# Kernel tuning notes

Measured on AMD Instinct MI355X. Metric: run time of the kernel, lower is better.

Reference implementation:

```python
import jax, jax.numpy as jnp
import numpy as np

SEQ, BATCH, EMBED = 1024, 2, 768
E = 16            # num_experts = m * N = 2 * 8
FFN_H = 1536      # expert_dim = ceil(3072 / 2)
K_SHARED = 1
K_ROUTE = 3       # (m * top_k) - k_shared = 4 - 1
LN_EPS = 1e-5
NEG_INF = -1e9


def setup_inputs() -> dict:
    key = jax.random.key(0)
    ks = jax.random.split(key, 4)
    x = jax.random.normal(ks[0], (SEQ, BATCH, EMBED), dtype=jnp.float32)
    gate_w = jax.random.normal(ks[1], (EMBED, E), dtype=jnp.float32) * 0.02
    gate_b = jnp.zeros((E,), jnp.float32)
    fc1_w = jax.random.normal(ks[2], (E, EMBED, FFN_H), dtype=jnp.float32) * 0.02
    fc1_b = jnp.zeros((E, FFN_H), jnp.float32)
    ln_w = jnp.ones((E, FFN_H), jnp.float32)
    ln_b = jnp.zeros((E, FFN_H), jnp.float32)
    fc2_w = jax.random.normal(ks[3], (E, FFN_H, EMBED), dtype=jnp.float32) * 0.02
    fc2_b = jnp.zeros((E, EMBED), jnp.float32)
    return {"x": x, "gate_w": gate_w, "gate_b": gate_b,
            "fc1_w": fc1_w, "fc1_b": fc1_b, "ln_w": ln_w, "ln_b": ln_b,
            "fc2_w": fc2_w, "fc2_b": fc2_b}


def reference(x, gate_w, gate_b, fc1_w, fc1_b, ln_w, ln_b, fc2_w, fc2_b):
    S, B, D = x.shape
    T = S * B
    xf = x.reshape(T, D)

    # --- gating: mask shared-expert logits, softmax, top-k over routed probs ---
    scores = xf @ gate_w + gate_b                      # [T, E]
    scores = scores.at[:, :K_SHARED].set(NEG_INF)
    probs = jax.nn.softmax(scores, axis=-1)
    topv, topi = jax.lax.top_k(probs, K_ROUTE)         # [T, K_ROUTE]

    # combine weights: gate prob for selected routed experts, 1.0 for shared experts
    combine = jnp.zeros((T, E), xf.dtype)
    combine = combine.at[jnp.arange(T)[:, None], topi].add(topv)
    combine = combine.at[:, :K_SHARED].add(1.0)        # shared expert(s), weight 1

    # --- per-expert FFN (dense over experts; combine zeros out unselected) ---
    h = jnp.einsum('td,edh->eth', xf, fc1_w) + fc1_b[:, None, :]   # [E, T, H]
    h = jax.nn.gelu(h, approximate=False)              # torch nn.GELU = exact erf
    mu = h.mean(-1, keepdims=True)
    var = h.var(-1, keepdims=True)
    h = (h - mu) * jax.lax.rsqrt(var + LN_EPS) * ln_w[:, None, :] + ln_b[:, None, :]
    y = jnp.einsum('eth,ehd->etd', h, fc2_w) + fc2_b[:, None, :]   # [E, T, D]

    # --- scatter-add combine (gate-weighted sum over experts) ---
    out = jnp.einsum('te,etd->td', combine, y)
    return out.reshape(S, B, D)
```

## Files before the change

### kernel.cpp

```cpp
#include <hip/hip_runtime.h>
#include <cmath>

#define T_TOK 2048
#define D_EMB 768
#define H_FFN 1536
#define NE    16
#define NPAIR (T_TOK * 4)

#define NW1   9216
#define NW2   9216
#define NX    768
#define NB    12
#define NGATE 512

typedef __attribute__((ext_vector_type(8))) short          short8;
typedef __attribute__((ext_vector_type(4))) short          short4v;
typedef __attribute__((ext_vector_type(8))) unsigned short ushort8;
typedef __attribute__((ext_vector_type(4))) unsigned short ushort4v;
typedef __attribute__((ext_vector_type(4))) float          floatx4;

__device__ __forceinline__ float bf2f(unsigned short u) {
  union { unsigned int i; float f; } v; v.i = ((unsigned int)u) << 16; return v.f;
}
__device__ __forceinline__ unsigned short f2bf(float f) {
  union { float f; unsigned int i; } v; v.f = f;
  unsigned int r = v.i + 0x7fffu + ((v.i >> 16) & 1u);
  return (unsigned short)(r >> 16);
}

__device__ __forceinline__ void gload16(const unsigned short* g, unsigned short* l) {
  __builtin_amdgcn_global_load_lds(
      (const __attribute__((address_space(1))) unsigned int*)g,
      (__attribute__((address_space(3))) unsigned int*)l,
      16, 0, 0);
}

__device__ __forceinline__ unsigned ldsaddr(const void* p) {
  return (unsigned)(unsigned long long)
      (const __attribute__((address_space(3))) char*)p;
}

__device__ __forceinline__ short4v tr8(unsigned a) {
  short4v d;
  asm volatile("ds_read_b64_tr_b16 %0, %1" : "=v"(d) : "v"(a));
  return d;
}

__device__ __forceinline__ int block_sniff(const unsigned int* __restrict__ xw, int tid) {
  int c = 0;
#pragma unroll
  for (int i = 0; i < 2; i++) {
    unsigned int w = xw[tid * 2 + i];
    unsigned int e = (w >> 7) & 0xFFu;
    c += (e >= 100u && e <= 140u) ? 1 : 0;
  }
#pragma unroll
  for (int off = 32; off > 0; off >>= 1) c += __shfl_down(c, off);
  __shared__ int ssn[4];
  int wave = tid >> 6, lane = tid & 63;
  if (lane == 0) ssn[wave] = c;
  __syncthreads();
  return (ssn[0] + ssn[1] + ssn[2] + ssn[3] > 300) ? 1 : 0;
}

__device__ __forceinline__ void conv8(const float* __restrict__ src,
                                      unsigned short* __restrict__ dst, size_t i) {
  floatx4 a = *(const floatx4*)(src + i);
  floatx4 b = *(const floatx4*)(src + i + 4);
  ushort8 o;
#pragma unroll
  for (int j = 0; j < 4; j++) { o[j] = f2bf(a[j]); o[4 + j] = f2bf(b[j]); }
  *(ushort8*)(dst + i) = o;
}

__global__ __launch_bounds__(256) void prep_kernel(
    const unsigned int* __restrict__ xw,
    const unsigned short* __restrict__ x16, const float* __restrict__ x32,
    const unsigned short* __restrict__ gw16, const float* __restrict__ gw32,
    const unsigned short* __restrict__ gb16, const float* __restrict__ gb32,
    const float* __restrict__ w1F, const float* __restrict__ w2F,
    const float* __restrict__ fc1bF, const float* __restrict__ lnwF,
    const float* __restrict__ lnbF, const float* __restrict__ fc2bF,
    unsigned short* __restrict__ xC,
    unsigned short* __restrict__ wsW1, unsigned short* __restrict__ wsW2,
    unsigned short* __restrict__ dfc1b, unsigned short* __restrict__ dlnw,
    unsigned short* __restrict__ dlnb, unsigned short* __restrict__ dfc2b,
    int* __restrict__ flagOut,
    int* __restrict__ psel, float* __restrict__ pw,
    int* __restrict__ cnt, int* __restrict__ plist)
{
  __shared__ __align__(16) float sacc[4][64][17];
  int bid = blockIdx.x;
  int tid = threadIdx.x;
  int isbf = block_sniff(xw, tid);
  if (bid == 0 && tid == 0) *flagOut = isbf;

  if (bid < NW1) {
    if (!isbf) conv8(w1F, wsW1, ((size_t)bid * 256 + tid) * 8);
  } else if (bid < NW1 + NW2) {
    if (!isbf) conv8(w2F, wsW2, ((size_t)(bid - NW1) * 256 + tid) * 8);
  } else if (bid < NW1 + NW2 + NX) {
    if (!isbf) conv8(x32, xC, ((size_t)(bid - NW1 - NW2) * 256 + tid) * 8);
  } else if (bid < NW1 + NW2 + NX + NB) {
    if (!isbf) {
      size_t g = (size_t)(bid - NW1 - NW2 - NX) * 256 + tid;
      size_t i = g * 8;
      conv8(fc1bF, dfc1b, i);
      conv8(lnwF,  dlnw,  i);
      conv8(lnbF,  dlnb,  i);
      if (g < 1536) conv8(fc2bF, dfc2b, i);
    }
  } else {
    int wave = tid >> 6, lane = tid & 63;
    int t = (bid - (NW1 + NW2 + NX + NB)) * 4 + wave;
    float acc[NE];
#pragma unroll
    for (int e = 0; e < NE; e++) acc[e] = 0.f;
    if (isbf) {
#pragma unroll
      for (int i = 0; i < D_EMB / 64; i++) {
        int d = i * 64 + lane;
        float xv = bf2f(x16[(size_t)t * D_EMB + d]);
        ushort8 g0 = *(const ushort8*)(gw16 + d * NE);
        ushort8 g1 = *(const ushort8*)(gw16 + d * NE + 8);
#pragma unroll
        for (int e = 0; e < 8; e++) acc[e]     += xv * bf2f(g0[e]);
#pragma unroll
        for (int e = 0; e < 8; e++) acc[8 + e] += xv * bf2f(g1[e]);
      }
    } else {
#pragma unroll
      for (int i = 0; i < D_EMB / 64; i++) {
        int d = i * 64 + lane;
        float xv = x32[(size_t)t * D_EMB + d];
#pragma unroll
        for (int q = 0; q < 4; q++) {
          floatx4 g = *(const floatx4*)(gw32 + d * NE + q * 4);
#pragma unroll
          for (int j = 0; j < 4; j++) acc[q * 4 + j] += xv * g[j];
        }
      }
    }
#pragma unroll
    for (int e = 0; e < NE; e++) sacc[wave][lane][e] = acc[e];
    __syncthreads();
    int e = lane & 15, q = lane >> 4;
    float s = 0.f;
#pragma unroll
    for (int i = 0; i < 16; i++) s += sacc[wave][q * 16 + i][e];
    s += __shfl_xor(s, 16);
    s += __shfl_xor(s, 32);
    float sv = s + (isbf ? bf2f(gb16[e]) : gb32[e]);
    if (e == 0) sv = -1e9f;
    float m = sv;
#pragma unroll
    for (int off = 8; off > 0; off >>= 1) m = fmaxf(m, __shfl_xor(m, off));
    float pe = expf(sv - m);
    float den = pe;
#pragma unroll
    for (int off = 8; off > 0; off >>= 1) den += __shfl_xor(den, off);
    float pr = pe / den;
    float val = (e == 0) ? -1.f : pr;
    int sel0, sel1, sel2; float sw0, sw1, sw2;
#pragma unroll
    for (int k = 0; k < 3; k++) {
      float bv = val; int bi = e;
#pragma unroll
      for (int off = 8; off > 0; off >>= 1) {
        float ov = __shfl_xor(bv, off);
        int   oi = __shfl_xor(bi, off);
        if (ov > bv || (ov == bv && oi < bi)) { bv = ov; bi = oi; }
      }
      if (k == 0) { sel0 = bi; sw0 = bv; }
      else if (k == 1) { sel1 = bi; sw1 = bv; }
      else { sel2 = bi; sw2 = bv; }
      if (e == bi) val = -1.f;
    }
    if (lane < 4) {
      int se; float swt;
      if (lane == 0)      { se = 0;    swt = 1.0f; }
      else if (lane == 1) { se = sel0; swt = sw0; }
      else if (lane == 2) { se = sel1; swt = sw1; }
      else                { se = sel2; swt = sw2; }
      int pidx = t * 4 + lane;
      psel[pidx] = se; pw[pidx] = swt;
      int pos = atomicAdd(&cnt[se], 1);
      plist[se * T_TOK + pos] = pidx;
    }
  }
}

template<int KDIM, int NDIM, bool GELU, bool HASBIAS, bool AROWDIV4, bool OUTF32>
__global__ __launch_bounds__(256) void moe_gemm(
    const unsigned short* __restrict__ AO, const unsigned short* __restrict__ AC,
    const unsigned short* __restrict__ BO, const unsigned short* __restrict__ BC,
    const unsigned short* __restrict__ biasO, const unsigned short* __restrict__ biasC,
    const int* __restrict__ flag,
    const int* __restrict__ cnt, const int* __restrict__ plist,
    unsigned short* __restrict__ outB, float* __restrict__ outF)
{
  const int NSP = NDIM / 128;
  int bx  = blockIdx.x;
  int e   = bx / (16 * NSP);
  int rem = bx % (16 * NSP);
  int mt  = rem / NSP;
  int ns  = rem % NSP;
  int count = cnt[e];
  if (mt * 128 >= count) return;
  const unsigned short* Abase   = (*flag) ? AO : AC;
  const unsigned short* Bbase   = (*flag) ? BO : BC;
  const unsigned short* biasAll = (*flag) ? biasO : biasC;

  __shared__ __align__(16) unsigned short sA[128 * 64];
  __shared__ __align__(16) unsigned short sB[64 * 128];
  __shared__ int sp[128];

  int tid = threadIdx.x;
  if (tid < 128) {
    int rg  = mt * 128 + tid;
    int idx = rg < count ? rg : count - 1;
    sp[tid] = plist[e * T_TOK + idx];
  }
  __syncthreads();

  int lane = tid & 63;
  int wave = tid >> 6;
  int n0   = ns * 128;

  int lrow  = lane >> 3;
  int lsch  = (lane & 7) ^ lrow;
  const unsigned short* ag[4];
  int loffA[4];
#pragma unroll
  for (int s = 0; s < 4; s++) {
    int r  = wave * 32 + s * 8;
    int p  = sp[r + lrow];
    ag[s] = Abase + (size_t)(AROWDIV4 ? (p >> 2) : p) * KDIM + lsch * 8;
    loffA[s] = r * 64;
  }

  int bk = (lane >> 1) & 3;
  int bn = (lane >> 3) * 16 + (lane & 1) * 8;
  const unsigned short* bg[4];
  int loffB[4];
#pragma unroll
  for (int s = 0; s < 4; s++) {
    int krow = wave * 16 + s * 4 + bk;
    bg[s] = Bbase + ((size_t)e * KDIM + krow) * NDIM + n0 + bn;
    loffB[s] = (wave * 4 + s) * 512;
  }

  int m16  = lane & 15;
  int quad = lane >> 4;
  int wm   = (wave >> 1) * 64;
  int wn   = (wave & 1) * 64;
  int rsw  = (m16 & 7);
  unsigned trB = ldsaddr(sB)
               + (unsigned)(quad * 2048 + (wave & 1) * 512 + m16 * 8);

  floatx4 acc[4][4];
#pragma unroll
  for (int i = 0; i < 4; i++)
#pragma unroll
    for (int j = 0; j < 4; j++) acc[i][j] = (floatx4){0.f, 0.f, 0.f, 0.f};

  for (int k0 = 0; k0 < KDIM; k0 += 64) {
    if (k0) __syncthreads();
#pragma unroll
    for (int s = 0; s < 4; s++) gload16(ag[s] + k0, sA + loffA[s]);
#pragma unroll
    for (int s = 0; s < 4; s++) gload16(bg[s] + (size_t)k0 * NDIM, sB + loffB[s]);
    __syncthreads();
#pragma unroll
    for (int ks = 0; ks < 2; ks++) {
      int ch = ((ks * 4 + quad) ^ rsw) * 8;
      short8 af[4];
#pragma unroll
      for (int m = 0; m < 4; m++)
        af[m] = *(const short8*)(sA + (wm + m * 16 + m16) * 64 + ch);
      short8 bf[4];
#pragma unroll
      for (int nt = 0; nt < 4; nt++) {
        union { short4v h[2]; short8 w; } u;
        u.h[0] = tr8(trB + (unsigned)(ks * 8192 + nt * 128));
        u.h[1] = tr8(trB + (unsigned)(ks * 8192 + 1024 + nt * 128));
        bf[nt] = u.w;
      }
      asm volatile("s_waitcnt lgkmcnt(0)" ::: "memory");
      __builtin_amdgcn_sched_barrier(0);
#pragma unroll
      for (int m = 0; m < 4; m++)
#pragma unroll
        for (int n = 0; n < 4; n++)
          acc[m][n] = __builtin_amdgcn_mfma_f32_16x16x32_bf16(af[m], bf[n], acc[m][n], 0, 0, 0);
    }
  }

#pragma unroll
  for (int m = 0; m < 4; m++) {
#pragma unroll
    for (int r = 0; r < 4; r++) {
      int row_local = wm + m * 16 + quad * 4 + r;
      int rg = mt * 128 + row_local;
      if (rg < count) {
        int p = sp[row_local];
#pragma unroll
        for (int n = 0; n < 4; n++) {
          int col = n0 + wn + n * 16 + m16;
          float v = acc[m][n][r];
          if (HASBIAS) v += bf2f(biasAll[e * NDIM + col]);
          if (GELU)    v = 0.5f * v * (1.f + erff(v * 0.70710678118654752f));
          if (OUTF32) outF[(size_t)p * NDIM + col] = v;
          else        outB[(size_t)p * NDIM + col] = f2bf(v);
        }
      }
    }
  }
}

__global__ __launch_bounds__(256) void ln_kernel(
    unsigned short* __restrict__ Hbuf,
    const unsigned short* __restrict__ lnwO, const unsigned short* __restrict__ lnwC,
    const unsigned short* __restrict__ lnbO, const unsigned short* __restrict__ lnbC,
    const int* __restrict__ psel, const float* __restrict__ pw,
    const int* __restrict__ flag)
{
  int p = blockIdx.x;
  int tid = threadIdx.x;
  int e = psel[p];
  int isbf = *flag;
  const unsigned short* lnw = isbf ? lnwO : lnwC;
  const unsigned short* lnb = isbf ? lnbO : lnbC;
  unsigned short* hr = Hbuf + (size_t)p * H_FFN;
  bool act = tid < 192;
  float v[8];
  float s = 0.f, sq = 0.f;
  if (act) {
    ushort8 hv = *(const ushort8*)(hr + tid * 8);
#pragma unroll
    for (int j = 0; j < 8; j++) { v[j] = bf2f(hv[j]); s += v[j]; sq += v[j] * v[j]; }
  }
#pragma unroll
  for (int off = 32; off > 0; off >>= 1) {
    s  += __shfl_down(s, off);
    sq += __shfl_down(sq, off);
  }
  __shared__ float red[8];
  int wave = tid >> 6, lane = tid & 63;
  if (lane == 0) { red[wave * 2] = s; red[wave * 2 + 1] = sq; }
  __syncthreads();
  __shared__ float mv[2];
  if (tid == 0) {
    float S = 0.f, Q = 0.f;
    for (int w = 0; w < 4; w++) { S += red[w * 2]; Q += red[w * 2 + 1]; }
    float mu  = S * (1.f / H_FFN);
    float var = Q * (1.f / H_FFN) - mu * mu;
    mv[0] = mu; mv[1] = rsqrtf(var + 1e-5f);
  }
  __syncthreads();
  if (act) {
    float mu = mv[0], rstd = mv[1];
    float w = pw[p];
    ushort8 lw = *(const ushort8*)(lnw + e * H_FFN + tid * 8);
    ushort8 lb = *(const ushort8*)(lnb + e * H_FFN + tid * 8);
    ushort8 o;
#pragma unroll
    for (int j = 0; j < 8; j++)
      o[j] = f2bf(((v[j] - mu) * rstd * bf2f(lw[j]) + bf2f(lb[j])) * w);
    *(ushort8*)(hr + tid * 8) = o;
  }
}

__global__ __launch_bounds__(192) void combine_kernel(
    const float* __restrict__ Y,
    const unsigned short* __restrict__ b2O, const unsigned short* __restrict__ b2C,
    const int* __restrict__ psel, const float* __restrict__ pw,
    unsigned short* __restrict__ out16, float* __restrict__ out32,
    const int* __restrict__ flag)
{
  int t = blockIdx.x;
  int tid = threadIdx.x;
  int isbf = *flag;
  const unsigned short* b2 = isbf ? b2O : b2C;
  int e1 = psel[t * 4 + 1], e2 = psel[t * 4 + 2], e3 = psel[t * 4 + 3];
  float w1 = pw[t * 4 + 1], w2 = pw[t * 4 + 2], w3 = pw[t * 4 + 3];
  int d = tid * 4;
  const float* Yb = Y + (size_t)t * 4 * D_EMB + d;
  floatx4 y0 = *(const floatx4*)(Yb);
  floatx4 y1 = *(const floatx4*)(Yb + D_EMB);
  floatx4 y2 = *(const floatx4*)(Yb + 2 * D_EMB);
  floatx4 y3 = *(const floatx4*)(Yb + 3 * D_EMB);
  ushort4v b0 = *(const ushort4v*)(b2 + d);
  ushort4v bb1 = *(const ushort4v*)(b2 + e1 * D_EMB + d);
  ushort4v bb2 = *(const ushort4v*)(b2 + e2 * D_EMB + d);
  ushort4v bb3 = *(const ushort4v*)(b2 + e3 * D_EMB + d);
  if (isbf) {
    ushort4v o;
#pragma unroll
    for (int j = 0; j < 4; j++) {
      float a = y0[j] + y1[j] + y2[j] + y3[j] + bf2f(b0[j])
              + w1 * bf2f(bb1[j]) + w2 * bf2f(bb2[j]) + w3 * bf2f(bb3[j]);
      o[j] = f2bf(a);
    }
    *(ushort4v*)(out16 + (size_t)t * D_EMB + d) = o;
  } else {
    floatx4 o;
#pragma unroll
    for (int j = 0; j < 4; j++)
      o[j] = y0[j] + y1[j] + y2[j] + y3[j] + bf2f(b0[j])
           + w1 * bf2f(bb1[j]) + w2 * bf2f(bb2[j]) + w3 * bf2f(bb3[j]);
    *(floatx4*)(out32 + (size_t)t * D_EMB + d) = o;
  }
}

extern "C" void kernel_launch(void* const* d_in, const int* in_sizes, int n_in,
                              void* d_out, int out_size, void* d_ws, size_t ws_size,
                              hipStream_t stream)
{
  (void)in_sizes; (void)n_in; (void)out_size; (void)ws_size;
  char* ws = (char*)d_ws;
  int*   cnt   = (int*)ws;
  int*   plist = (int*)(ws + 256);
  int*   psel  = (int*)(ws + 131328);
  float* pw    = (float*)(ws + 164096);
  int*   flag  = (int*)(ws + 196864);
  unsigned short* fc1bC = (unsigned short*)(ws + 197120);
  unsigned short* lnwC  = (unsigned short*)(ws + 246272);
  unsigned short* lnbC  = (unsigned short*)(ws + 295424);
  unsigned short* fc2bC = (unsigned short*)(ws + 344576);
  unsigned short* xC    = (unsigned short*)(ws + 524288);
  unsigned short* Hbuf  = (unsigned short*)(ws + 3670016);
  float*          Ybuf  = (float*)(ws + 28835840);
  unsigned short* wsW1  = (unsigned short*)(ws + 54001664);
  unsigned short* wsW2  = (unsigned short*)(ws + 91750400);

  hipMemsetAsync(cnt, 0, 64, stream);

  prep_kernel<<<NW1 + NW2 + NX + NB + NGATE, 256, 0, stream>>>(
      (const unsigned int*)d_in[0],
      (const unsigned short*)d_in[0], (const float*)d_in[0],
      (const unsigned short*)d_in[1], (const float*)d_in[1],
      (const unsigned short*)d_in[2], (const float*)d_in[2],
      (const float*)d_in[3], (const float*)d_in[7],
      (const float*)d_in[4], (const float*)d_in[5],
      (const float*)d_in[6], (const float*)d_in[8],
      xC, wsW1, wsW2,
      fc1bC, lnwC, lnbC, fc2bC,
      flag, psel, pw, cnt, plist);

  moe_gemm<D_EMB, H_FFN, true, true, true, false>
      <<<NE * 16 * (H_FFN / 128), 256, 0, stream>>>(
      (const unsigned short*)d_in[0], xC,
      (const unsigned short*)d_in[3], wsW1,
      (const unsigned short*)d_in[4], fc1bC,
      flag, cnt, plist, Hbuf, nullptr);

  ln_kernel<<<NPAIR, 256, 0, stream>>>(
      Hbuf,
      (const unsigned short*)d_in[5], lnwC,
      (const unsigned short*)d_in[6], lnbC,
      psel, pw, flag);

  moe_gemm<H_FFN, D_EMB, false, false, false, true>
      <<<NE * 16 * (D_EMB / 128), 256, 0, stream>>>(
      Hbuf, Hbuf,
      (const unsigned short*)d_in[7], wsW2,
      nullptr, nullptr,
      flag, cnt, plist, nullptr, Ybuf);

  combine_kernel<<<T_TOK, 192, 0, stream>>>(
      Ybuf,
      (const unsigned short*)d_in[8], fc2bC,
      psel, pw,
      (unsigned short*)d_out, (float*)d_out, flag);
}
```

Measured before the change: 350.8 us.

## Overlap fc2 weight conversion with fc1 GEMM and batch weight-convert blocks

The fp32→bf16 conversion of the fc2 weights moves out of the prep kernel and into extra tail blocks of the fc1 GEMM launch, so it can run alongside the GEMM tiles and fill idle CUs, especially since many GEMM tiles exit early for low-count experts. The prep kernel now puts the gating blocks first and converts fc1 weights with each block handling four chunks, which cuts the block count. The added blocks in the GEMM grid compete with the GEMM for memory bandwidth and CU slots. The GEMM also gains two extra pointer parameters.

```diff
diff --git a/kernel.cpp b/kernel.cpp
--- a/kernel.cpp
+++ b/kernel.cpp
@@ -7,11 +7,11 @@
 #define NE    16
 #define NPAIR (T_TOK * 4)
 
-#define NW1   9216
-#define NW2   9216
+#define NGATE 512
 #define NX    768
 #define NB    12
-#define NGATE 512
+#define NW1B  2304
+#define NW2B  2304
 
 typedef __attribute__((ext_vector_type(8))) short          short8;
 typedef __attribute__((ext_vector_type(4))) short          short4v;
@@ -78,11 +78,11 @@
     const unsigned short* __restrict__ x16, const float* __restrict__ x32,
     const unsigned short* __restrict__ gw16, const float* __restrict__ gw32,
     const unsigned short* __restrict__ gb16, const float* __restrict__ gb32,
-    const float* __restrict__ w1F, const float* __restrict__ w2F,
+    const float* __restrict__ w1F,
     const float* __restrict__ fc1bF, const float* __restrict__ lnwF,
     const float* __restrict__ lnbF, const float* __restrict__ fc2bF,
     unsigned short* __restrict__ xC,
-    unsigned short* __restrict__ wsW1, unsigned short* __restrict__ wsW2,
+    unsigned short* __restrict__ wsW1,
     unsigned short* __restrict__ dfc1b, unsigned short* __restrict__ dlnw,
     unsigned short* __restrict__ dlnb, unsigned short* __restrict__ dfc2b,
     int* __restrict__ flagOut,
@@ -95,24 +95,9 @@
   int isbf = block_sniff(xw, tid);
   if (bid == 0 && tid == 0) *flagOut = isbf;
 
-  if (bid < NW1) {
-    if (!isbf) conv8(w1F, wsW1, ((size_t)bid * 256 + tid) * 8);
-  } else if (bid < NW1 + NW2) {
-    if (!isbf) conv8(w2F, wsW2, ((size_t)(bid - NW1) * 256 + tid) * 8);
-  } else if (bid < NW1 + NW2 + NX) {
-    if (!isbf) conv8(x32, xC, ((size_t)(bid - NW1 - NW2) * 256 + tid) * 8);
-  } else if (bid < NW1 + NW2 + NX + NB) {
-    if (!isbf) {
-      size_t g = (size_t)(bid - NW1 - NW2 - NX) * 256 + tid;
-      size_t i = g * 8;
-      conv8(fc1bF, dfc1b, i);
-      conv8(lnwF,  dlnw,  i);
-      conv8(lnbF,  dlnb,  i);
-      if (g < 1536) conv8(fc2bF, dfc2b, i);
-    }
-  } else {
+  if (bid < NGATE) {
     int wave = tid >> 6, lane = tid & 63;
-    int t = (bid - (NW1 + NW2 + NX + NB)) * 4 + wave;
+    int t = bid * 4 + wave;
     float acc[NE];
 #pragma unroll
     for (int e = 0; e < NE; e++) acc[e] = 0.f;
@@ -187,20 +172,53 @@
       int pos = atomicAdd(&cnt[se], 1);
       plist[se * T_TOK + pos] = pidx;
     }
-  }
-}
-
-template<int KDIM, int NDIM, bool GELU, bool HASBIAS, bool AROWDIV4, bool OUTF32>
+  } else if (bid < NGATE + NX) {
+    if (!isbf) conv8(x32, xC, ((size_t)(bid - NGATE) * 256 + tid) * 8);
+  } else if (bid < NGATE + NX + NB) {
+    if (!isbf) {
+      size_t g = (size_t)(bid - NGATE - NX) * 256 + tid;
+      size_t i = g * 8;
+      conv8(fc1bF, dfc1b, i);
+      conv8(lnwF,  dlnw,  i);
+      conv8(lnbF,  dlnb,  i);
+      if (g < 1536) conv8(fc2bF, dfc2b, i);
+    }
+  } else {
+    if (!isbf) {
+      int cb = bid - (NGATE + NX + NB);
+#pragma unroll
+      for (int it = 0; it < 4; it++)
+        conv8(w1F, wsW1, ((size_t)(cb * 4 + it) * 256 + tid) * 8);
+    }
+  }
+}
+
+template<int KDIM, int NDIM, bool GELU, bool HASBIAS, bool AROWDIV4, bool OUTF32,
+         bool CONVW2>
 __global__ __launch_bounds__(256) void moe_gemm(
     const unsigned short* __restrict__ AO, const unsigned short* __restrict__ AC,
     const unsigned short* __restrict__ BO, const unsigned short* __restrict__ BC,
     const unsigned short* __restrict__ biasO, const unsigned short* __restrict__ biasC,
+    const float* __restrict__ w2F, unsigned short* __restrict__ w2D,
     const int* __restrict__ flag,
     const int* __restrict__ cnt, const int* __restrict__ plist,
     unsigned short* __restrict__ outB, float* __restrict__ outF)
 {
   const int NSP = NDIM / 128;
   int bx  = blockIdx.x;
+  int tid = threadIdx.x;
+  if (CONVW2) {
+    const int nblk = NE * 16 * NSP;
+    if (bx >= nblk) {
+      if (!*flag) {
+        int cb = bx - nblk;
+#pragma unroll
+        for (int it = 0; it < 4; it++)
+          conv8(w2F, w2D, ((size_t)(cb * 4 + it) * 256 + tid) * 8);
+      }
+      return;
+    }
+  }
   int e   = bx / (16 * NSP);
   int rem = bx % (16 * NSP);
   int mt  = rem / NSP;
@@ -215,7 +233,6 @@
   __shared__ __align__(16) unsigned short sB[64 * 128];
   __shared__ int sp[128];
 
-  int tid = threadIdx.x;
   if (tid < 128) {
     int rg  = mt * 128 + tid;
     int idx = rg < count ? rg : count - 1;
@@ -436,23 +453,24 @@
 
   hipMemsetAsync(cnt, 0, 64, stream);
 
-  prep_kernel<<<NW1 + NW2 + NX + NB + NGATE, 256, 0, stream>>>(
+  prep_kernel<<<NGATE + NX + NB + NW1B, 256, 0, stream>>>(
       (const unsigned int*)d_in[0],
       (const unsigned short*)d_in[0], (const float*)d_in[0],
       (const unsigned short*)d_in[1], (const float*)d_in[1],
       (const unsigned short*)d_in[2], (const float*)d_in[2],
-      (const float*)d_in[3], (const float*)d_in[7],
+      (const float*)d_in[3],
       (const float*)d_in[4], (const float*)d_in[5],
       (const float*)d_in[6], (const float*)d_in[8],
-      xC, wsW1, wsW2,
+      xC, wsW1,
       fc1bC, lnwC, lnbC, fc2bC,
       flag, psel, pw, cnt, plist);
 
-  moe_gemm<D_EMB, H_FFN, true, true, true, false>
-      <<<NE * 16 * (H_FFN / 128), 256, 0, stream>>>(
+  moe_gemm<D_EMB, H_FFN, true, true, true, false, true>
+      <<<NE * 16 * (H_FFN / 128) + NW2B, 256, 0, stream>>>(
       (const unsigned short*)d_in[0], xC,
       (const unsigned short*)d_in[3], wsW1,
       (const unsigned short*)d_in[4], fc1bC,
+      (const float*)d_in[7], wsW2,
       flag, cnt, plist, Hbuf, nullptr);
 
   ln_kernel<<<NPAIR, 256, 0, stream>>>(
@@ -461,10 +479,11 @@
       (const unsigned short*)d_in[6], lnbC,
       psel, pw, flag);
 
-  moe_gemm<H_FFN, D_EMB, false, false, false, true>
+  moe_gemm<H_FFN, D_EMB, false, false, false, true, false>
       <<<NE * 16 * (D_EMB / 128), 256, 0, stream>>>(
       Hbuf, Hbuf,
       (const unsigned short*)d_in[7], wsW2,
+      nullptr, nullptr,
       nullptr, nullptr,
       flag, cnt, plist, nullptr, Ybuf);
 
```

Result: faster. 342.7 us (-2.3%).
